# Optimization experiments

Measured on AMD Instinct MI355X. Metric: run time of the kernel, lower is better.

The kernel has to match this reference:

```python
import jax, jax.numpy as jnp
import numpy as np
from math import factorial, sqrt

L = 8
RCUT = 5.0
PI = 3.14159  # literal used in the torch module's Ylm normalization
N_POINTS = 4194304


def powcmplx(zr, zi, n):
    # Faithful port, including the n>2 recurrence that uses the *updated*
    # real part when forming the imaginary part (as in the source).
    if n == 0:
        return jnp.ones_like(zr), jnp.zeros_like(zr)
    if n == 1:
        return zr, zi
    if n == 2:
        return zr * zr - zi * zi, 2.0 * zr * zi
    r, im = zr, zi
    for _ in range(2, n + 1):
        r = zr * r - zi * im
        im = zr * im + zi * r  # uses updated r, matching the source exactly
    return r, im


def _forward(pos):
    norms = jnp.sqrt(jnp.sum(pos * pos, axis=1))
    valid = norms > 0
    mask = valid.astype(pos.dtype)
    safe = jnp.where(valid, norms, 1.0)
    # cosine_cutoff uses the true pi (acos trick in the source)
    cut = 0.5 * (jnp.cos(norms * (jnp.pi / RCUT)) + 1.0)
    cut = jnp.where(norms > RCUT, 0.0, cut) * mask  # mask replaces boolean row-select
    xp_r = -0.5 * pos[:, 0]
    xp_i = -0.5 * pos[:, 1]
    xm_r = 0.5 * pos[:, 0]
    xm_i = -0.5 * pos[:, 1]
    x0 = pos[:, 2]
    n_out = (L + 1) ** 2
    vals = [jnp.zeros((), pos.dtype)] * n_out
    i = 0
    for l in range(L + 1):
        w_l = cut / safe ** l * sqrt((2 * l + 1) / 4 / PI)  # per-point weight for this l
        for M in range(-l, 1):
            m = abs(M)
            sr = jnp.zeros_like(x0)
            si = jnp.zeros_like(x0)
            for p in range(l + 1):
                q = p - m
                s = l - p - q
                if q >= 0 and s >= 0:
                    z1r, z1i = powcmplx(xp_r, xp_i, p)
                    z2r, z2i = powcmplx(xm_r, xm_i, q)
                    zr = z1r ** 2 - z2i ** 2      # faithful to source (squared terms)
                    zi = z1r * z2i + z1i * z2r
                    c = 1.0 / (factorial(p) * factorial(q) * factorial(s))
                    sr = sr + zr * x0 * c          # source multiplies by x0 (x0**s is unused there)
                    si = si + zi * x0 * c
            f = sqrt(factorial(l + m) * factorial(l - m))
            w = f * w_l
            clm_r = jnp.sum(sr * w)
            clm_i = jnp.sum(si * w)
            if m == 0:
                vals[i] = clm_r
            else:
                fac = sqrt(2.0) * (-1) ** m
                vals[i] = fac * clm_i
                vals[i + 2 * m] = fac * clm_r
            i += 1
        i += l
    return jnp.stack(vals).reshape(-1, 1)


def setup_inputs() -> dict:
    key = jax.random.key(0)
    pos = jax.random.normal(key, (N_POINTS, 3), dtype=jnp.float32) * 2.0
    return {"pos": pos}


def reference(pos):
    return _forward(pos)
```

## Files before the change

### kernel.cpp

```cpp
#include <hip/hip_runtime.h>
#include <math.h>


typedef float f32x2 __attribute__((ext_vector_type(2)));

#define NL 8
#define NACC 45
#define NBLK 1024
#define NTHR 256

__device__ __forceinline__ f32x2 sp(float v) { return f32x2{v, v}; }

__device__ __forceinline__ f32x2 pkfma(f32x2 a, f32x2 b, f32x2 c) {
    return __builtin_elementwise_fma(a, b, c);
}

__device__ __forceinline__ float waveReduce(float v) {
    v += __shfl_down(v, 32);
    v += __shfl_down(v, 16);
    v += __shfl_down(v, 8);
    v += __shfl_down(v, 4);
    v += __shfl_down(v, 2);
    v += __shfl_down(v, 1);
    return v;
}

__device__ __forceinline__ void point_body(float x, float y, float z,
                                           float* __restrict__ acc0,
                                           f32x2* __restrict__ accp) {
    const float FACT[9] = {1.f, 1.f, 2.f, 6.f, 24.f, 120.f, 720.f, 5040.f, 40320.f};

    const float r2 = x * x + y * y + z * z;
    const bool valid = r2 > 0.0f;
    const float inv0 = __builtin_amdgcn_rsqf(r2);
    const float norm = r2 * inv0;
    float cut = 0.5f * (__cosf(norm * 0.6283185307179586f) + 1.0f);
    cut = (r2 > 25.0f) ? 0.0f : cut;
    cut = valid ? cut : 0.0f;
    const float inv = valid ? inv0 : 1.0f;
    const float x0c = z * cut;

    const f32x2 w  = { -0.5f * x,  0.5f * x };
    const f32x2 wi = { -0.5f * y, -0.5f * y };

    f32x2 zr[9], zi[9];
    zr[0] = sp(1.f); zi[0] = sp(0.f);
    zr[1] = w;       zi[1] = wi;
    zr[2] = w * w - wi * wi;
    zi[2] = (w + w) * wi;
    {
        f32x2 cr = zr[2];
        f32x2 ci = w * wi + wi * cr;
#pragma unroll
        for (int k = 3; k <= NL; ++k) {
            const f32x2 nr = w * cr - wi * ci;
            const f32x2 ni = w * ci + wi * nr;
            cr = nr; ci = ni;
            zr[k] = nr; zi[k] = ni;
        }
    }

    float aa[9], bb[9], cc[9], dd[9], sqa[9];
#pragma unroll
    for (int p = 0; p <= NL; ++p) {
        aa[p] = zr[p].x;
        cc[p] = zr[p].y;
        bb[p] = zi[p].x;
        dd[p] = zi[p].y;
        sqa[p] = aa[p] * aa[p];
    }

    float h[9];
    h[0] = x0c;
#pragma unroll
    for (int l = 1; l <= NL; ++l) h[l] = h[l - 1] * inv;

    {
        float Y0[5];
#pragma unroll
        for (int p = 0; p <= 4; ++p) {
            const float cpq = 1.0f / (FACT[p] * FACT[p]);
            Y0[p] = fmaf(-dd[p], dd[p], sqa[p]) * cpq;
        }
#pragma unroll
        for (int l = 0; l <= NL; ++l) {
            float sr = 0.f;
#pragma unroll
            for (int p = 0; p <= 4; ++p) {
                if (2 * p <= l) {
                    const float is = 1.0f / FACT[l - 2 * p];
                    sr = fmaf(Y0[p], is, sr);
                }
            }
            acc0[l] = fmaf(sr, h[l], acc0[l]);
        }
    }

#pragma unroll
    for (int m = 1; m <= NL; ++m) {
        f32x2 Y[9];
#pragma unroll
        for (int p = 0; p <= NL; ++p) {
            if (p >= m && 2 * p - m <= NL) {
                const int q = p - m;
                const float cpq = 1.0f / (FACT[p] * FACT[q]);
                const float bc = bb[p] * cc[q];
                const f32x2 A = { -dd[q], aa[p] };
                const f32x2 B = {  dd[q], dd[q] };
                const f32x2 C = { sqa[p], bc };
                Y[p] = pkfma(A, B, C) * sp(cpq);
            }
        }
#pragma unroll
        for (int l = m; l <= NL; ++l) {
            f32x2 s = sp(0.f);
#pragma unroll
            for (int p = 0; p <= NL; ++p) {
                if (p >= m && 2 * p - m <= l) {
                    const float is = 1.0f / FACT[l - 2 * p + m];
                    s = pkfma(Y[p], sp(is), s);
                }
            }
            const int ai = l * (l - 1) / 2 + (m - 1);
            accp[ai] = pkfma(s, sp(h[l]), accp[ai]);
        }
    }
}

__global__ __launch_bounds__(256, 2)
void sht_main(const float* __restrict__ pos, float* __restrict__ ws, int n) {
    float acc0[9];
    f32x2 accp[36];
#pragma unroll
    for (int i = 0; i < 9; ++i) acc0[i] = 0.f;
#pragma unroll
    for (int i = 0; i < 36; ++i) accp[i] = sp(0.f);

    const int t = blockIdx.x * NTHR + threadIdx.x;
    const int nthreads = NBLK * NTHR;
    const int nchunks = (n / 8 + nthreads - 1) / nthreads;

    for (int c = 0; c < nchunks; ++c) {
        const int idx = (c * nthreads + t) * 8;
        float xs[8], ys[8], zs[8];
        if (idx + 8 <= n) {
            const float4* p4 = reinterpret_cast<const float4*>(pos + (size_t)3 * idx);
            const float4 q0 = p4[0], q1 = p4[1], q2 = p4[2];
            const float4 q3 = p4[3], q4 = p4[4], q5 = p4[5];
            xs[0] = q0.x; ys[0] = q0.y; zs[0] = q0.z;
            xs[1] = q0.w; ys[1] = q1.x; zs[1] = q1.y;
            xs[2] = q1.z; ys[2] = q1.w; zs[2] = q2.x;
            xs[3] = q2.y; ys[3] = q2.z; zs[3] = q2.w;
            xs[4] = q3.x; ys[4] = q3.y; zs[4] = q3.z;
            xs[5] = q3.w; ys[5] = q4.x; zs[5] = q4.y;
            xs[6] = q4.z; ys[6] = q4.w; zs[6] = q5.x;
            xs[7] = q5.y; ys[7] = q5.z; zs[7] = q5.w;
        } else {
#pragma unroll
            for (int k = 0; k < 8; ++k) {
                const int i = idx + k;
                const bool ok = i < n;
                xs[k] = ok ? pos[3 * i + 0] : 0.f;
                ys[k] = ok ? pos[3 * i + 1] : 0.f;
                zs[k] = ok ? pos[3 * i + 2] : 0.f;
            }
        }
#pragma unroll
        for (int k = 0; k < 8; ++k)
            point_body(xs[k], ys[k], zs[k], acc0, accp);
    }

    __shared__ float red[81][5];
    const int lane = threadIdx.x & 63;
    const int wave = threadIdx.x >> 6;

#pragma unroll
    for (int l = 0; l <= NL; ++l) {
        float vr = waveReduce(acc0[l]);
        if (lane == 0) red[l * l + l][wave] = vr;
    }
#pragma unroll
    for (int m = 1; m <= NL; ++m) {
#pragma unroll
        for (int l = m; l <= NL; ++l) {
            const int ai = l * (l - 1) / 2 + (m - 1);
            float vr = waveReduce(accp[ai].x);
            if (lane == 0) red[l * l + l + m][wave] = vr;
            float vi = waveReduce(accp[ai].y);
            if (lane == 0) red[l * l + l - m][wave] = vi;
        }
    }
    __syncthreads();

    if ((int)threadIdx.x < 81) {
        float s = 0.f;
#pragma unroll
        for (int w = 0; w < 4; ++w) s += red[threadIdx.x][w];
        ws[(size_t)threadIdx.x * NBLK + blockIdx.x] = s;
    }
}

__device__ double dfact(int nn) {
    double r = 1.0;
    for (int i = 2; i <= nn; ++i) r *= (double)i;
    return r;
}

__global__ __launch_bounds__(256)
void sht_finalize(const float* __restrict__ ws, float* __restrict__ out) {
    const int j = blockIdx.x;
    const int t = threadIdx.x;
    float s = 0.f;
#pragma unroll
    for (int k = 0; k < NBLK / 256; ++k)
        s += ws[(size_t)j * NBLK + k * 256 + t];
    s = waveReduce(s);

    __shared__ float red[4];
    const int lane = t & 63, wave = t >> 6;
    if (lane == 0) red[wave] = s;
    __syncthreads();
    if (t == 0) {
        float tot = red[0] + red[1] + red[2] + red[3];
        int l = 0;
        while ((l + 1) * (l + 1) <= j) ++l;
        const int M = j - l * l - l;
        const int m = (M < 0) ? -M : M;
        double sc = sqrt(dfact(l + m) * dfact(l - m)) *
                    sqrt((double)(2 * l + 1) / (4.0 * 3.14159));
        if (m > 0) sc *= sqrt(2.0) * ((m & 1) ? -1.0 : 1.0);
        out[j] = (float)((double)tot * sc);
    }
}

extern "C" void kernel_launch(void* const* d_in, const int* in_sizes, int n_in,
                              void* d_out, int out_size, void* d_ws, size_t ws_size,
                              hipStream_t stream) {
    const float* pos = (const float*)d_in[0];
    const int npts = in_sizes[0] / 3;
    float* ws = (float*)d_ws;
    float* out = (float*)d_out;

    sht_main<<<NBLK, NTHR, 0, stream>>>(pos, ws, npts);
    sht_finalize<<<81, 256, 0, stream>>>(ws, out);
}
```

Measured before the change: 138.5 us.

## Split harmonic orders across two block groups to cut per-thread register load

The main kernel now launches twice as many blocks. One half accumulates orders m=0..2 and the other m=3..8, each processing all points with a templated point body that only computes the powers and accumulators its slice needs. This lowers per-thread accumulator count, aiming to relieve register pressure and spills and to raise occupancy. In exchange, positions are read twice and the shared setup work (norm, cutoff, power recurrences) is duplicated across both halves.

```diff
diff --git a/kernel.cpp b/kernel.cpp
--- a/kernel.cpp
+++ b/kernel.cpp
@@ -5,7 +5,6 @@
 typedef float f32x2 __attribute__((ext_vector_type(2)));
 
 #define NL 8
-#define NACC 45
 #define NBLK 1024
 #define NTHR 256
 
@@ -25,9 +24,23 @@
     return v;
 }
 
+__device__ constexpr int tri_off(int m1, int m) {
+    int o = 0;
+    for (int k = m1; k < m; ++k) o += 9 - k;
+    return o;
+}
+__device__ constexpr int npairs(int m1, int mhi) {
+    int o = 0;
+    for (int k = m1; k <= mhi; ++k) o += 9 - k;
+    return o;
+}
+
+template <int MLO, int MHI>
 __device__ __forceinline__ void point_body(float x, float y, float z,
                                            float* __restrict__ acc0,
                                            f32x2* __restrict__ accp) {
+    constexpr int PMAX = (8 + MHI) / 2;
+    constexpr int M1 = (MLO < 1) ? 1 : MLO;
     const float FACT[9] = {1.f, 1.f, 2.f, 6.f, 24.f, 120.f, 720.f, 5040.f, 40320.f};
 
     const float r2 = x * x + y * y + z * z;
@@ -43,7 +56,7 @@
     const f32x2 w  = { -0.5f * x,  0.5f * x };
     const f32x2 wi = { -0.5f * y, -0.5f * y };
 
-    f32x2 zr[9], zi[9];
+    f32x2 zr[PMAX + 1], zi[PMAX + 1];
     zr[0] = sp(1.f); zi[0] = sp(0.f);
     zr[1] = w;       zi[1] = wi;
     zr[2] = w * w - wi * wi;
@@ -52,7 +65,7 @@
         f32x2 cr = zr[2];
         f32x2 ci = w * wi + wi * cr;
 #pragma unroll
-        for (int k = 3; k <= NL; ++k) {
+        for (int k = 3; k <= PMAX; ++k) {
             const f32x2 nr = w * cr - wi * ci;
             const f32x2 ni = w * ci + wi * nr;
             cr = nr; ci = ni;
@@ -60,9 +73,9 @@
         }
     }
 
-    float aa[9], bb[9], cc[9], dd[9], sqa[9];
-#pragma unroll
-    for (int p = 0; p <= NL; ++p) {
+    float aa[PMAX + 1], bb[PMAX + 1], cc[PMAX + 1], dd[PMAX + 1], sqa[PMAX + 1];
+#pragma unroll
+    for (int p = 0; p <= PMAX; ++p) {
         aa[p] = zr[p].x;
         cc[p] = zr[p].y;
         bb[p] = zi[p].x;
@@ -75,7 +88,7 @@
 #pragma unroll
     for (int l = 1; l <= NL; ++l) h[l] = h[l - 1] * inv;
 
-    {
+    if constexpr (MLO == 0) {
         float Y0[5];
 #pragma unroll
         for (int p = 0; p <= 4; ++p) {
@@ -97,10 +110,10 @@
     }
 
 #pragma unroll
-    for (int m = 1; m <= NL; ++m) {
-        f32x2 Y[9];
-#pragma unroll
-        for (int p = 0; p <= NL; ++p) {
+    for (int m = M1; m <= MHI; ++m) {
+        f32x2 Y[PMAX + 1];
+#pragma unroll
+        for (int p = 0; p <= PMAX; ++p) {
             if (p >= m && 2 * p - m <= NL) {
                 const int q = p - m;
                 const float cpq = 1.0f / (FACT[p] * FACT[q]);
@@ -115,28 +128,37 @@
         for (int l = m; l <= NL; ++l) {
             f32x2 s = sp(0.f);
 #pragma unroll
-            for (int p = 0; p <= NL; ++p) {
+            for (int p = 0; p <= PMAX; ++p) {
                 if (p >= m && 2 * p - m <= l) {
                     const float is = 1.0f / FACT[l - 2 * p + m];
                     s = pkfma(Y[p], sp(is), s);
                 }
             }
-            const int ai = l * (l - 1) / 2 + (m - 1);
+            const int ai = tri_off(M1, m) + (l - m);
             accp[ai] = pkfma(s, sp(h[l]), accp[ai]);
         }
     }
 }
 
-__global__ __launch_bounds__(256, 2)
-void sht_main(const float* __restrict__ pos, float* __restrict__ ws, int n) {
-    float acc0[9];
-    f32x2 accp[36];
-#pragma unroll
-    for (int i = 0; i < 9; ++i) acc0[i] = 0.f;
-#pragma unroll
-    for (int i = 0; i < 36; ++i) accp[i] = sp(0.f);
-
-    const int t = blockIdx.x * NTHR + threadIdx.x;
+template <int MLO, int MHI>
+__device__ __forceinline__ void run_slice(const float* __restrict__ pos,
+                                          float* __restrict__ ws, int n,
+                                          int bid) {
+    constexpr int M1 = (MLO < 1) ? 1 : MLO;
+    constexpr int NP = npairs(M1, MHI);
+    constexpr int BASE = (MLO == 0) ? 9 : 0;
+    constexpr int NLOC = BASE + 2 * NP;
+
+    float acc0[(MLO == 0) ? 9 : 1];
+    f32x2 accp[NP];
+    if constexpr (MLO == 0) {
+#pragma unroll
+        for (int i = 0; i < 9; ++i) acc0[i] = 0.f;
+    }
+#pragma unroll
+    for (int i = 0; i < NP; ++i) accp[i] = sp(0.f);
+
+    const int t = bid * NTHR + (int)threadIdx.x;
     const int nthreads = NBLK * NTHR;
     const int nchunks = (n / 8 + nthreads - 1) / nthreads;
 
@@ -167,37 +189,60 @@
         }
 #pragma unroll
         for (int k = 0; k < 8; ++k)
-            point_body(xs[k], ys[k], zs[k], acc0, accp);
-    }
-
-    __shared__ float red[81][5];
+            point_body<MLO, MHI>(xs[k], ys[k], zs[k], acc0, accp);
+    }
+
+    __shared__ float red[NLOC][5];
     const int lane = threadIdx.x & 63;
     const int wave = threadIdx.x >> 6;
 
-#pragma unroll
-    for (int l = 0; l <= NL; ++l) {
-        float vr = waveReduce(acc0[l]);
-        if (lane == 0) red[l * l + l][wave] = vr;
-    }
-#pragma unroll
-    for (int m = 1; m <= NL; ++m) {
+    if constexpr (MLO == 0) {
+#pragma unroll
+        for (int l = 0; l <= NL; ++l) {
+            float vr = waveReduce(acc0[l]);
+            if (lane == 0) red[l][wave] = vr;
+        }
+    }
+#pragma unroll
+    for (int m = M1; m <= MHI; ++m) {
 #pragma unroll
         for (int l = m; l <= NL; ++l) {
-            const int ai = l * (l - 1) / 2 + (m - 1);
-            float vr = waveReduce(accp[ai].x);
-            if (lane == 0) red[l * l + l + m][wave] = vr;
-            float vi = waveReduce(accp[ai].y);
-            if (lane == 0) red[l * l + l - m][wave] = vi;
+            const int pi = tri_off(M1, m) + (l - m);
+            float vr = waveReduce(accp[pi].x);
+            if (lane == 0) red[BASE + 2 * pi + 0][wave] = vr;
+            float vi = waveReduce(accp[pi].y);
+            if (lane == 0) red[BASE + 2 * pi + 1][wave] = vi;
         }
     }
     __syncthreads();
 
-    if ((int)threadIdx.x < 81) {
+    if ((int)threadIdx.x < NLOC) {
+        const int tid = threadIdx.x;
         float s = 0.f;
 #pragma unroll
-        for (int w = 0; w < 4; ++w) s += red[threadIdx.x][w];
-        ws[(size_t)threadIdx.x * NBLK + blockIdx.x] = s;
-    }
+        for (int w = 0; w < 4; ++w) s += red[tid][w];
+        int j;
+        if (MLO == 0 && tid < 9) {
+            j = tid * tid + tid;
+        } else {
+            int r = tid - BASE;
+            int pairIdx = r >> 1;
+            const bool im = r & 1;
+            int m = M1, rem = pairIdx;
+            while (rem >= 9 - m) { rem -= 9 - m; ++m; }
+            const int l = m + rem;
+            j = l * l + l + (im ? -m : m);
+        }
+        ws[(size_t)j * NBLK + bid] = s;
+    }
+}
+
+__global__ __launch_bounds__(256, 2)
+void sht_main(const float* __restrict__ pos, float* __restrict__ ws, int n) {
+    if (blockIdx.x < NBLK)
+        run_slice<0, 2>(pos, ws, n, blockIdx.x);
+    else
+        run_slice<3, 8>(pos, ws, n, blockIdx.x - NBLK);
 }
 
 __device__ double dfact(int nn) {
@@ -241,6 +286,6 @@
     float* ws = (float*)d_ws;
     float* out = (float*)d_out;
 
-    sht_main<<<NBLK, NTHR, 0, stream>>>(pos, ws, npts);
+    sht_main<<<2 * NBLK, NTHR, 0, stream>>>(pos, ws, npts);
     sht_finalize<<<81, 256, 0, stream>>>(ws, out);
 }
```

Result: slower. 141.8 us (+2.4%).
